# Kernel optimization log

Hardware: AMD Instinct MI355X
Metric: run time of the kernel (lower is better)

## Reference

```python
import jax, jax.numpy as jnp
import numpy as np

N_NODES = 100000
N_EDGES = 1600000
NIN = 128
NHID = 128
N_GRAPHS = 1024


def _gcn_conv(x, src, dst, norm, W, b, n_nodes):
    """PyG-style GCNConv: linear (no bias) -> normalized scatter-add -> + bias."""
    xw = x @ W                                   # [N, out]
    msg = xw[src] * norm[:, None]                # gather + edge-normalize, [E', out]
    out = jax.ops.segment_sum(msg, dst, num_segments=n_nodes)
    return out + b


def _gcn_norm(edge_index, n_nodes):
    """Add self-loops and compute symmetric deg^{-1/2} normalization per edge."""
    loops = jnp.arange(n_nodes, dtype=edge_index.dtype)
    src = jnp.concatenate([edge_index[0], loops])
    dst = jnp.concatenate([edge_index[1], loops])
    deg = jax.ops.segment_sum(jnp.ones_like(dst, dtype=jnp.float32), dst,
                              num_segments=n_nodes)
    deg_isqrt = jnp.where(deg > 0, jax.lax.rsqrt(jnp.maximum(deg, 1.0)), 0.0)
    norm = deg_isqrt[src] * deg_isqrt[dst]
    return src, dst, norm


def setup_inputs() -> dict:
    key = jax.random.key(0)
    ks = jax.random.split(key, 8)
    x = jax.random.normal(ks[0], (N_NODES, NIN), dtype=jnp.float32)
    edge_index = jax.random.randint(ks[1], (2, N_EDGES), 0, N_NODES, dtype=jnp.int64)
    batch = jnp.sort(jax.random.randint(ks[2], (N_NODES,), 0, N_GRAPHS, dtype=jnp.int64))
    s_in = 1.0 / np.sqrt(NIN)
    s_h = 1.0 / np.sqrt(NHID)
    return {
        "x": x,
        "edge_index": edge_index,
        "batch": batch,
        "W1": jax.random.normal(ks[3], (NIN, NHID), dtype=jnp.float32) * s_in,
        "b1": jnp.zeros((NHID,), dtype=jnp.float32),
        "W2": jax.random.normal(ks[4], (NHID, NHID), dtype=jnp.float32) * s_h,
        "b2": jnp.zeros((NHID,), dtype=jnp.float32),
        "W3": jax.random.normal(ks[5], (NHID, NHID), dtype=jnp.float32) * s_h,
        "b3": jnp.zeros((NHID,), dtype=jnp.float32),
        "Wfc": jax.random.normal(ks[6], (NHID, 1), dtype=jnp.float32) * s_h,
        "bfc": jnp.zeros((1,), dtype=jnp.float32),
    }


def reference(x, edge_index, batch, W1, b1, W2, b2, W3, b3, Wfc, bfc):
    n_nodes = x.shape[0]
    src, dst, norm = _gcn_norm(edge_index, n_nodes)
    h = jax.nn.relu(_gcn_conv(x, src, dst, norm, W1, b1, n_nodes))
    h = jax.nn.relu(_gcn_conv(h, src, dst, norm, W2, b2, n_nodes))
    h = jax.nn.relu(_gcn_conv(h, src, dst, norm, W3, b3, n_nodes))
    # global mean pool over graphs in the batch
    sums = jax.ops.segment_sum(h, batch, num_segments=N_GRAPHS)      # [G, NHID]
    cnts = jax.ops.segment_sum(jnp.ones((n_nodes,), dtype=h.dtype), batch,
                               num_segments=N_GRAPHS)
    pooled = sums / jnp.maximum(cnts, 1.0)[:, None]
    return pooled @ Wfc + bfc                                        # [G, 1]
```

## Files before the change

### kernel.cpp

```cpp
#include <hip/hip_runtime.h>

#define N_NODES   100000
#define N_EDGES   1600000
#define NFEAT     128
#define N_GRAPHS  1024

#define BSHIFT  8
#define BNODES  256
#define NBUCK   391
#define BCAP    4608
#define SC_EDGES 4096
#define SC_EPT   8
#define SC_BLOCKS 391
#define BD_EPT   18

#define WT_STRIDE 136
#define GEMM_BLOCKS 782

typedef unsigned int uint32;
typedef unsigned short ushort;
typedef __attribute__((ext_vector_type(8))) short short8;
typedef __attribute__((ext_vector_type(4))) float f32x4;

__device__ inline ushort f2b(float f) {
    uint32 x = __float_as_uint(f);
    uint32 r = x + 0x7fffu + ((x >> 16) & 1u);
    return (ushort)(r >> 16);
}
__device__ inline float blo(uint32 u) { return __uint_as_float(u << 16); }
__device__ inline float bhi(uint32 u) { return __uint_as_float(u & 0xffff0000u); }

__device__ inline short8 cvt8(const float* p) {
    float4 v0 = ((const float4*)p)[0];
    float4 v1 = ((const float4*)p)[1];
    short8 r;
    r[0] = (short)f2b(v0.x); r[1] = (short)f2b(v0.y);
    r[2] = (short)f2b(v0.z); r[3] = (short)f2b(v0.w);
    r[4] = (short)f2b(v1.x); r[5] = (short)f2b(v1.y);
    r[6] = (short)f2b(v1.z); r[7] = (short)f2b(v1.w);
    return r;
}

__global__ __launch_bounds__(256) void k_castw(const float* __restrict__ W1, const float* __restrict__ W2,
                                               const float* __restrict__ W3, ushort* __restrict__ WT,
                                               int* __restrict__ cur) {
    int i = blockIdx.x * blockDim.x + threadIdx.x;
    if (i < NBUCK) cur[i] = 0;
    if (i >= 3 * NFEAT * NFEAT) return;
    int l = i >> 14;
    int j = i & 16383;
    int n = j >> 7;
    int k = j & 127;
    const float* W = (l == 0) ? W1 : (l == 1) ? W2 : W3;
    WT[i] = f2b(W[k * NFEAT + n]);
}

struct SMemScatter {
    int hist[NBUCK], lofs[NBUCK], gbase[NBUCK];
    int wsum[4];
    uint32 sortedP[SC_EDGES];
    ushort sortedB[SC_EDGES];
};

__global__ __launch_bounds__(512) void k_phase1(const int* __restrict__ src, const int* __restrict__ dst,
                                                int* __restrict__ cur, uint32* __restrict__ bbuf,
                                                const float* __restrict__ A, const ushort* __restrict__ WTl,
                                                ushort* __restrict__ C, int M) {
    __shared__ __align__(16) char smem[NFEAT * WT_STRIDE * 2];
    int t = threadIdx.x;
    if (blockIdx.x < SC_BLOCKS) {
        SMemScatter& S = *(SMemScatter*)smem;
        int e0 = blockIdx.x * SC_EDGES;
        int total = N_EDGES - e0; if (total > SC_EDGES) total = SC_EDGES; if (total < 0) total = 0;
        for (int i = t; i < NBUCK; i += 512) S.hist[i] = 0;
        __syncthreads();
        uint32 val[SC_EPT];
        int    meta[SC_EPT];
        #pragma unroll
        for (int k = 0; k < SC_EPT; ++k) {
            int i = t + k * 512;
            meta[k] = -1;
            if (i < total) {
                int s = src[e0 + i], d = dst[e0 + i];
                int b = d >> BSHIFT;
                int tk = atomicAdd(&S.hist[b], 1);
                val[k] = ((uint32)(d & (BNODES - 1)) << 17) | (uint32)s;
                meta[k] = (b << 13) | tk;
            }
        }
        __syncthreads();
        int inc = 0, ts = 0, h0 = 0;
        if (t < 256) {
            int b0 = 2 * t, b1 = 2 * t + 1;
            h0 = (b0 < NBUCK) ? S.hist[b0] : 0;
            int h1 = (b1 < NBUCK) ? S.hist[b1] : 0;
            ts = h0 + h1;
            int lane = t & 63;
            inc = ts;
            #pragma unroll
            for (int d = 1; d < 64; d <<= 1) {
                int u = __shfl_up(inc, d, 64);
                if (lane >= d) inc += u;
            }
            if (lane == 63) S.wsum[t >> 6] = inc;
        }
        __syncthreads();
        if (t < 256) {
            int w = t >> 6;
            int wpre = 0;
            for (int i = 0; i < w; ++i) wpre += S.wsum[i];
            int run = wpre + inc - ts;
            int b0 = 2 * t, b1 = 2 * t + 1;
            int h1 = ts - h0;
            if (b0 < NBUCK) {
                S.lofs[b0] = run;
                if (h0) S.gbase[b0] = atomicAdd(&cur[b0], h0);
            }
            if (b1 < NBUCK) {
                S.lofs[b1] = run + h0;
                if (h1) S.gbase[b1] = atomicAdd(&cur[b1], h1);
            }
        }
        __syncthreads();
        #pragma unroll
        for (int k = 0; k < SC_EPT; ++k) {
            if (meta[k] >= 0) {
                int b = meta[k] >> 13;
                int p = S.lofs[b] + (meta[k] & 0x1FFF);
                S.sortedP[p] = val[k];
                S.sortedB[p] = (ushort)b;
            }
        }
        __syncthreads();
        for (int i = t; i < total; i += 512) {
            int b = S.sortedB[i];
            int addr = S.gbase[b] + (i - S.lofs[b]);
            if (addr < BCAP)
                bbuf[(size_t)b * BCAP + addr] = S.sortedP[i];
        }
    } else {
        ushort* sWT = (ushort*)smem;
        int gb = blockIdx.x - SC_BLOCKS;
        for (int i = t; i < NFEAT * 16; i += 512) {
            int n = i >> 4, c = i & 15;
            *(float4*)(sWT + n * WT_STRIDE + c * 8) = ((const float4*)WTl)[i];
        }
        int wave = t >> 6, lane = t & 63;
        int m0 = gb * 128 + wave * 16;
        int mRow = m0 + (lane & 15);
        if (mRow >= M) mRow = M - 1;
        int kg = lane >> 4;
        const float* Ap = A + (size_t)mRow * NFEAT + kg * 8;
        short8 a0 = cvt8(Ap);
        short8 a1 = cvt8(Ap + 32);
        short8 a2 = cvt8(Ap + 64);
        short8 a3 = cvt8(Ap + 96);
        __syncthreads();

        f32x4 acc[8];
        #pragma unroll
        for (int nt = 0; nt < 8; ++nt) acc[nt] = (f32x4){0.f, 0.f, 0.f, 0.f};
        #pragma unroll
        for (int nt = 0; nt < 8; ++nt) {
            int n = nt * 16 + (lane & 15);
            const short8* Bp = (const short8*)(sWT + n * WT_STRIDE + kg * 8);
            short8 b0 = Bp[0];
            short8 b1 = Bp[4];
            short8 b2 = Bp[8];
            short8 b3 = Bp[12];
            acc[nt] = __builtin_amdgcn_mfma_f32_16x16x32_bf16(a0, b0, acc[nt], 0, 0, 0);
            acc[nt] = __builtin_amdgcn_mfma_f32_16x16x32_bf16(a1, b1, acc[nt], 0, 0, 0);
            acc[nt] = __builtin_amdgcn_mfma_f32_16x16x32_bf16(a2, b2, acc[nt], 0, 0, 0);
            acc[nt] = __builtin_amdgcn_mfma_f32_16x16x32_bf16(a3, b3, acc[nt], 0, 0, 0);
        }
        __syncthreads();
        {
            int colBase = lane & 15;
            #pragma unroll
            for (int r = 0; r < 4; ++r) {
                int lr = wave * 16 + kg * 4 + r;
                #pragma unroll
                for (int nt = 0; nt < 8; ++nt)
                    sWT[lr * NFEAT + nt * 16 + colBase] = f2b(acc[nt][r]);
            }
        }
        __syncthreads();
        {
            int rowBase = gb * 128;
            const float4* sC4 = (const float4*)sWT;
            for (int i = t; i < 2048; i += 512) {
                int row = i >> 4;
                int gr = rowBase + row;
                if (gr < M) ((float4*)(C + (size_t)gr * NFEAT))[i & 15] = sC4[i];
            }
        }
    }
}

__global__ __launch_bounds__(256) void k_build(const uint32* __restrict__ bbuf, const int* __restrict__ cur,
                                               int* __restrict__ col, int* __restrict__ offsets,
                                               float* __restrict__ dinv) {
    int b = blockIdx.x;
    __shared__ int hist[BNODES], excl[BNODES];
    __shared__ int wsum[4], wtot[4];
    __shared__ int sorted[BCAP];
    __shared__ int sBase, sTotal;
    int t = threadIdx.x;
    {
        int pre = 0, tot = 0;
        #pragma unroll
        for (int q = 0; q < 2; ++q) {
            int i = 2 * t + q;
            if (i < NBUCK) {
                int v = cur[i]; if (v > BCAP) v = BCAP;
                tot += v;
                if (i < b) pre += v;
            }
        }
        int lane = t & 63, w = t >> 6;
        #pragma unroll
        for (int d = 32; d > 0; d >>= 1) { pre += __shfl_down(pre, d, 64); tot += __shfl_down(tot, d, 64); }
        if (lane == 0) { wsum[w] = pre; wtot[w] = tot; }
        __syncthreads();
        if (t == 0) {
            sBase = wsum[0] + wsum[1] + wsum[2] + wsum[3];
            sTotal = wtot[0] + wtot[1] + wtot[2] + wtot[3];
        }
        hist[t] = 0;
    }
    __syncthreads();
    int base = sBase;
    if (b == NBUCK - 1 && t == 0) offsets[N_NODES] = sTotal;
    int cnt = cur[b]; if (cnt > BCAP) cnt = BCAP;
    const uint32* reg = bbuf + (size_t)b * BCAP;

    uint32 val[BD_EPT];
    int    meta[BD_EPT];
    #pragma unroll
    for (int k = 0; k < BD_EPT; ++k) {
        int i = t + k * 256;
        meta[k] = -1;
        if (i < cnt) {
            uint32 p = reg[i];
            int node = p >> 17;
            int tk = atomicAdd(&hist[node], 1);
            val[k] = p & 0x1FFFF;
            meta[k] = (node << 16) | tk;
        }
    }
    __syncthreads();
    {
        int c = hist[t];
        int lane = t & 63, w = t >> 6;
        int inc = c;
        #pragma unroll
        for (int d = 1; d < 64; d <<= 1) {
            int u = __shfl_up(inc, d, 64);
            if (lane >= d) inc += u;
        }
        if (lane == 63) wsum[w] = inc;
        __syncthreads();
        int wpre = 0;
        for (int i = 0; i < w; ++i) wpre += wsum[i];
        int e = wpre + inc - c;
        excl[t] = e;
        int node = (b << BSHIFT) + t;
        if (node < N_NODES) {
            offsets[node] = base + e;
            dinv[node] = rsqrtf((float)(c + 1));
        }
    }
    __syncthreads();
    #pragma unroll
    for (int k = 0; k < BD_EPT; ++k) {
        if (meta[k] >= 0) {
            int node = meta[k] >> 16;
            sorted[excl[node] + (meta[k] & 0xFFFF)] = (int)val[k];
        }
    }
    __syncthreads();
    for (int i = t; i < cnt; i += 256) col[base + i] = sorted[i];
}

#define AGG_GROUP4 \
    int half = lane >> 4; \
    int fl = lane & 15; \
    float dn = dinv[n]; \
    int e0 = off[n], e1 = off[n + 1]; \
    int deg = e1 - e0; \
    int maxd = deg; \
    { int u16 = __shfl_xor(maxd, 16, 64); if (u16 > maxd) maxd = u16; \
      int u32 = __shfl_xor(maxd, 32, 64); if (u32 > maxd) maxd = u32; } \
    const uint4* XW4 = (const uint4*)XWu; \
    uint4 sv = XW4[(size_t)n * 16 + fl]; \
    float ws = dn * dn; \
    float a0 = ws * blo(sv.x), a1 = ws * bhi(sv.x); \
    float a2 = ws * blo(sv.y), a3 = ws * bhi(sv.y); \
    float a4 = ws * blo(sv.z), a5 = ws * bhi(sv.z); \
    float a6 = ws * blo(sv.w), a7 = ws * bhi(sv.w); \
    int cm = 0; float wm = 0.f; \
    if (fl < deg) { cm = col[e0 + fl]; wm = dn * dinv[cm]; } \
    for (int base = 0; base < maxd; base += 16) { \
        int nb = base + 16; \
        int cmn = 0; float wmn = 0.f; \
        if (nb + fl < deg) { cmn = col[e0 + nb + fl]; wmn = dn * dinv[cmn]; } \
        int lim = maxd - base; if (lim > 16) lim = 16; \
        for (int j = 0; j < lim; j += 8) { \
            uint4 u[8]; float w[8]; \
            _Pragma("unroll") \
            for (int p = 0; p < 8; ++p) { \
                int sl = (half << 4) + j + p; \
                int cc = __shfl(cm, sl, 64); \
                w[p] = __shfl(wm, sl, 64); \
                u[p] = XW4[(size_t)cc * 16 + fl]; \
            } \
            _Pragma("unroll") \
            for (int p = 0; p < 8; ++p) { \
                a0 = fmaf(w[p], blo(u[p].x), a0); a1 = fmaf(w[p], bhi(u[p].x), a1); \
                a2 = fmaf(w[p], blo(u[p].y), a2); a3 = fmaf(w[p], bhi(u[p].y), a3); \
                a4 = fmaf(w[p], blo(u[p].z), a4); a5 = fmaf(w[p], bhi(u[p].z), a5); \
                a6 = fmaf(w[p], blo(u[p].w), a6); a7 = fmaf(w[p], bhi(u[p].w), a7); \
            } \
        } \
        cm = cmn; wm = wmn; \
    }

__global__ __launch_bounds__(256) void k_agg_gemm(const uint32* __restrict__ XWu,
                                                  const int* __restrict__ col,
                                                  const int* __restrict__ off,
                                                  const float* __restrict__ dinv,
                                                  const float* __restrict__ bias,
                                                  const ushort* __restrict__ WTl,
                                                  ushort* __restrict__ C) {
    __shared__ __align__(16) ushort sA[16 * WT_STRIDE];
    int t = threadIdx.x;
    int lane = t & 63;
    int lw = t >> 6;
    int n = (blockIdx.x << 4) + (lw << 2) + (lane >> 4);
    AGG_GROUP4
    {
        float4 bb0 = ((const float4*)bias)[2 * fl];
        float4 bb1 = ((const float4*)bias)[2 * fl + 1];
        float r0 = fmaxf(a0 + bb0.x, 0.f), r1 = fmaxf(a1 + bb0.y, 0.f);
        float r2 = fmaxf(a2 + bb0.z, 0.f), r3 = fmaxf(a3 + bb0.w, 0.f);
        float r4 = fmaxf(a4 + bb1.x, 0.f), r5 = fmaxf(a5 + bb1.y, 0.f);
        float r6 = fmaxf(a6 + bb1.z, 0.f), r7 = fmaxf(a7 + bb1.w, 0.f);
        uint4 o;
        o.x = (uint32)f2b(r0) | ((uint32)f2b(r1) << 16);
        o.y = (uint32)f2b(r2) | ((uint32)f2b(r3) << 16);
        o.z = (uint32)f2b(r4) | ((uint32)f2b(r5) << 16);
        o.w = (uint32)f2b(r6) | ((uint32)f2b(r7) << 16);
        int lrow = (lw << 2) + half;
        *(uint4*)(sA + lrow * WT_STRIDE + fl * 8) = o;
    }
    __syncthreads();
    {
        const short8* Ap = (const short8*)(sA + fl * WT_STRIDE + half * 8);
        short8 af0 = Ap[0];
        short8 af1 = Ap[4];
        short8 af2 = Ap[8];
        short8 af3 = Ap[12];
        f32x4 acc[2];
        acc[0] = (f32x4){0.f, 0.f, 0.f, 0.f};
        acc[1] = (f32x4){0.f, 0.f, 0.f, 0.f};
        #pragma unroll
        for (int q = 0; q < 2; ++q) {
            int nt = lw * 2 + q;
            const short8* Bp = (const short8*)(WTl + (nt * 16 + fl) * NFEAT + half * 8);
            short8 b0 = Bp[0];
            short8 b1 = Bp[4];
            short8 b2 = Bp[8];
            short8 b3 = Bp[12];
            acc[q] = __builtin_amdgcn_mfma_f32_16x16x32_bf16(af0, b0, acc[q], 0, 0, 0);
            acc[q] = __builtin_amdgcn_mfma_f32_16x16x32_bf16(af1, b1, acc[q], 0, 0, 0);
            acc[q] = __builtin_amdgcn_mfma_f32_16x16x32_bf16(af2, b2, acc[q], 0, 0, 0);
            acc[q] = __builtin_amdgcn_mfma_f32_16x16x32_bf16(af3, b3, acc[q], 0, 0, 0);
        }
        __syncthreads();
        #pragma unroll
        for (int q = 0; q < 2; ++q) {
            int nt = lw * 2 + q;
            #pragma unroll
            for (int r = 0; r < 4; ++r)
                sA[(half * 4 + r) * NFEAT + nt * 16 + fl] = f2b(acc[q][r]);
        }
    }
    __syncthreads();
    {
        int row = t >> 4;
        float4 v = ((const float4*)sA)[t];
        ((float4*)(C + (size_t)((blockIdx.x << 4) + row) * NFEAT))[t & 15] = v;
    }
}

__global__ __launch_bounds__(256) void k_agg_fc(const uint32* __restrict__ XWu, const int* __restrict__ col,
                                                const int* __restrict__ off, const float* __restrict__ dinv,
                                                const float* __restrict__ bias, const float* __restrict__ Wfc,
                                                float* __restrict__ nodeS) {
    int wid = (blockIdx.x * blockDim.x + threadIdx.x) >> 6;
    int lane = threadIdx.x & 63;
    int n = (wid << 2) + (lane >> 4);
    if (n >= N_NODES) return;
    AGG_GROUP4
    float4 bb0 = ((const float4*)bias)[2 * fl];
    float4 bb1 = ((const float4*)bias)[2 * fl + 1];
    float4 wf0 = ((const float4*)Wfc)[2 * fl];
    float4 wf1 = ((const float4*)Wfc)[2 * fl + 1];
    float s = fmaxf(a0 + bb0.x, 0.f) * wf0.x + fmaxf(a1 + bb0.y, 0.f) * wf0.y
            + fmaxf(a2 + bb0.z, 0.f) * wf0.z + fmaxf(a3 + bb0.w, 0.f) * wf0.w
            + fmaxf(a4 + bb1.x, 0.f) * wf1.x + fmaxf(a5 + bb1.y, 0.f) * wf1.y
            + fmaxf(a6 + bb1.z, 0.f) * wf1.z + fmaxf(a7 + bb1.w, 0.f) * wf1.w;
    s += __shfl_xor(s, 8, 64);
    s += __shfl_xor(s, 4, 64);
    s += __shfl_xor(s, 2, 64);
    s += __shfl_xor(s, 1, 64);
    if (fl == 0) nodeS[n] = s;
}

__device__ inline int lower_bound_dev(const int* a, int n, int key) {
    int lo = 0, hi = n;
    while (lo < hi) {
        int mid = (lo + hi) >> 1;
        if (a[mid] < key) lo = mid + 1; else hi = mid;
    }
    return lo;
}

__global__ __launch_bounds__(256) void k_pool(const float* __restrict__ nodeS, const int* __restrict__ batch,
                                              const float* __restrict__ bfc, float* __restrict__ out) {
    int g = blockIdx.x;
    int t = threadIdx.x;
    int lo = lower_bound_dev(batch, N_NODES, g);
    int hi = lower_bound_dev(batch, N_NODES, g + 1);
    float s = 0.f;
    for (int i = lo + t; i < hi; i += 256) s += nodeS[i];
    for (int d = 32; d > 0; d >>= 1) s += __shfl_down(s, d, 64);
    __shared__ float ws[4];
    int lane = t & 63, w = t >> 6;
    if (lane == 0) ws[w] = s;
    __syncthreads();
    if (t == 0) {
        float tot = ws[0] + ws[1] + ws[2] + ws[3];
        float cnt = (float)(hi - lo);
        out[g] = tot / fmaxf(cnt, 1.0f) + bfc[0];
    }
}

extern "C" void kernel_launch(void* const* d_in, const int* in_sizes, int n_in,
                              void* d_out, int out_size, void* d_ws, size_t ws_size,
                              hipStream_t stream) {
    const float* x    = (const float*)d_in[0];
    const int*   ei   = (const int*)d_in[1];
    const int*   batch= (const int*)d_in[2];
    const float* W1   = (const float*)d_in[3];
    const float* b1   = (const float*)d_in[4];
    const float* W2   = (const float*)d_in[5];
    const float* b2   = (const float*)d_in[6];
    const float* W3   = (const float*)d_in[7];
    const float* b3   = (const float*)d_in[8];
    const float* Wfc  = (const float*)d_in[9];
    const float* bfc  = (const float*)d_in[10];
    float* out = (float*)d_out;

    const int* src = ei;
    const int* dst = ei + N_EDGES;

    char* p = (char*)d_ws;
    auto carve = [&](size_t bytes) { void* r = (void*)p; p += (bytes + 255) & ~(size_t)255; return r; };
    int*    cur       = (int*)   carve(sizeof(int) * NBUCK);
    uint32* bbuf      = (uint32*)carve(sizeof(uint32) * (size_t)NBUCK * BCAP);
    float*  dinv      = (float*) carve(sizeof(float) * N_NODES);
    int*    offsets   = (int*)   carve(sizeof(int) * (N_NODES + 1));
    int*    col       = (int*)   carve(sizeof(int) * N_EDGES);
    ushort* XW        = (ushort*)carve(sizeof(short) * (size_t)N_NODES * NFEAT);
    ushort* XW2       = (ushort*)carve(sizeof(short) * (size_t)N_NODES * NFEAT);
    ushort* WT        = (ushort*)carve(sizeof(short) * 3 * NFEAT * NFEAT);
    float*  nodeS     = (float*) carve(sizeof(float) * N_NODES);

    const int aggBlocks = N_NODES / 16;

    k_castw<<<(3 * NFEAT * NFEAT + 255) / 256, 256, 0, stream>>>(W1, W2, W3, WT, cur);
    k_phase1<<<SC_BLOCKS + GEMM_BLOCKS, 512, 0, stream>>>(src, dst, cur, bbuf, x, WT, XW, N_NODES);
    k_build<<<NBUCK, 256, 0, stream>>>(bbuf, cur, col, offsets, dinv);

    k_agg_gemm<<<aggBlocks, 256, 0, stream>>>((const uint32*)XW, col, offsets, dinv, b1,
                                              WT + NFEAT * NFEAT, XW2);
    k_agg_gemm<<<aggBlocks, 256, 0, stream>>>((const uint32*)XW2, col, offsets, dinv, b2,
                                              WT + 2 * NFEAT * NFEAT, XW);
    k_agg_fc<<<aggBlocks, 256, 0, stream>>>((const uint32*)XW, col, offsets, dinv, b3, Wfc, nodeS);

    k_pool<<<N_GRAPHS, 256, 0, stream>>>(nodeS, batch, bfc, out);
}
```

Baseline: 351.4 us.

## Replace bucketed two-pass CSR build with atomic degree count, scan and scatter

Builds the CSR adjacency a different way. The old path did a shared-memory bucket sort into a staging buffer followed by per-bucket local sorting. The new path counts degrees with global atomics, does a two-kernel prefix scan to get offsets and cursors, then places each edge with an atomic cursor increment. This removes the staging buffer, the shared-memory sorts and the capacity clamp. In exchange it adds random-address global atomics per edge, two more kernel launches, and a nondeterministic neighbor order within each node.

```diff
diff --git a/kernel.cpp b/kernel.cpp
--- a/kernel.cpp
+++ b/kernel.cpp
@@ -5,14 +5,10 @@
 #define NFEAT     128
 #define N_GRAPHS  1024
 
-#define BSHIFT  8
-#define BNODES  256
 #define NBUCK   391
-#define BCAP    4608
 #define SC_EDGES 4096
 #define SC_EPT   8
 #define SC_BLOCKS 391
-#define BD_EPT   18
 
 #define WT_STRIDE 136
 #define GEMM_BLOCKS 782
@@ -43,9 +39,9 @@
 
 __global__ __launch_bounds__(256) void k_castw(const float* __restrict__ W1, const float* __restrict__ W2,
                                                const float* __restrict__ W3, ushort* __restrict__ WT,
-                                               int* __restrict__ cur) {
+                                               int* __restrict__ deg) {
     int i = blockIdx.x * blockDim.x + threadIdx.x;
-    if (i < NBUCK) cur[i] = 0;
+    if (i < N_NODES) deg[i] = 0;
     if (i >= 3 * NFEAT * NFEAT) return;
     int l = i >> 14;
     int j = i & 16383;
@@ -55,91 +51,20 @@
     WT[i] = f2b(W[k * NFEAT + n]);
 }
 
-struct SMemScatter {
-    int hist[NBUCK], lofs[NBUCK], gbase[NBUCK];
-    int wsum[4];
-    uint32 sortedP[SC_EDGES];
-    ushort sortedB[SC_EDGES];
-};
-
 __global__ __launch_bounds__(512) void k_phase1(const int* __restrict__ src, const int* __restrict__ dst,
-                                                int* __restrict__ cur, uint32* __restrict__ bbuf,
+                                                int* __restrict__ deg,
                                                 const float* __restrict__ A, const ushort* __restrict__ WTl,
                                                 ushort* __restrict__ C, int M) {
-    __shared__ __align__(16) char smem[NFEAT * WT_STRIDE * 2];
+    __shared__ __align__(16) ushort sWT[NFEAT * WT_STRIDE];
     int t = threadIdx.x;
     if (blockIdx.x < SC_BLOCKS) {
-        SMemScatter& S = *(SMemScatter*)smem;
         int e0 = blockIdx.x * SC_EDGES;
-        int total = N_EDGES - e0; if (total > SC_EDGES) total = SC_EDGES; if (total < 0) total = 0;
-        for (int i = t; i < NBUCK; i += 512) S.hist[i] = 0;
-        __syncthreads();
-        uint32 val[SC_EPT];
-        int    meta[SC_EPT];
         #pragma unroll
         for (int k = 0; k < SC_EPT; ++k) {
-            int i = t + k * 512;
-            meta[k] = -1;
-            if (i < total) {
-                int s = src[e0 + i], d = dst[e0 + i];
-                int b = d >> BSHIFT;
-                int tk = atomicAdd(&S.hist[b], 1);
-                val[k] = ((uint32)(d & (BNODES - 1)) << 17) | (uint32)s;
-                meta[k] = (b << 13) | tk;
-            }
-        }
-        __syncthreads();
-        int inc = 0, ts = 0, h0 = 0;
-        if (t < 256) {
-            int b0 = 2 * t, b1 = 2 * t + 1;
-            h0 = (b0 < NBUCK) ? S.hist[b0] : 0;
-            int h1 = (b1 < NBUCK) ? S.hist[b1] : 0;
-            ts = h0 + h1;
-            int lane = t & 63;
-            inc = ts;
-            #pragma unroll
-            for (int d = 1; d < 64; d <<= 1) {
-                int u = __shfl_up(inc, d, 64);
-                if (lane >= d) inc += u;
-            }
-            if (lane == 63) S.wsum[t >> 6] = inc;
-        }
-        __syncthreads();
-        if (t < 256) {
-            int w = t >> 6;
-            int wpre = 0;
-            for (int i = 0; i < w; ++i) wpre += S.wsum[i];
-            int run = wpre + inc - ts;
-            int b0 = 2 * t, b1 = 2 * t + 1;
-            int h1 = ts - h0;
-            if (b0 < NBUCK) {
-                S.lofs[b0] = run;
-                if (h0) S.gbase[b0] = atomicAdd(&cur[b0], h0);
-            }
-            if (b1 < NBUCK) {
-                S.lofs[b1] = run + h0;
-                if (h1) S.gbase[b1] = atomicAdd(&cur[b1], h1);
-            }
-        }
-        __syncthreads();
-        #pragma unroll
-        for (int k = 0; k < SC_EPT; ++k) {
-            if (meta[k] >= 0) {
-                int b = meta[k] >> 13;
-                int p = S.lofs[b] + (meta[k] & 0x1FFF);
-                S.sortedP[p] = val[k];
-                S.sortedB[p] = (ushort)b;
-            }
-        }
-        __syncthreads();
-        for (int i = t; i < total; i += 512) {
-            int b = S.sortedB[i];
-            int addr = S.gbase[b] + (i - S.lofs[b]);
-            if (addr < BCAP)
-                bbuf[(size_t)b * BCAP + addr] = S.sortedP[i];
+            int i = e0 + t + k * 512;
+            if (i < N_EDGES) atomicAdd(&deg[dst[i]], 1);
         }
     } else {
-        ushort* sWT = (ushort*)smem;
         int gb = blockIdx.x - SC_BLOCKS;
         for (int i = t; i < NFEAT * 16; i += 512) {
             int n = i >> 4, c = i & 15;
@@ -197,89 +122,79 @@
     }
 }
 
-__global__ __launch_bounds__(256) void k_build(const uint32* __restrict__ bbuf, const int* __restrict__ cur,
-                                               int* __restrict__ col, int* __restrict__ offsets,
+__global__ __launch_bounds__(256) void k_scan1(const int* __restrict__ deg, int* __restrict__ bsum) {
+    int node = blockIdx.x * 256 + threadIdx.x;
+    int d = (node < N_NODES) ? deg[node] : 0;
+    int lane = threadIdx.x & 63, w = threadIdx.x >> 6;
+    #pragma unroll
+    for (int s = 32; s > 0; s >>= 1) d += __shfl_down(d, s, 64);
+    __shared__ int ws[4];
+    if (lane == 0) ws[w] = d;
+    __syncthreads();
+    if (threadIdx.x == 0) bsum[blockIdx.x] = ws[0] + ws[1] + ws[2] + ws[3];
+}
+
+__global__ __launch_bounds__(256) void k_scan2(const int* __restrict__ deg, const int* __restrict__ bsum,
+                                               int* __restrict__ offsets, int* __restrict__ cursor,
                                                float* __restrict__ dinv) {
-    int b = blockIdx.x;
-    __shared__ int hist[BNODES], excl[BNODES];
+    int b = blockIdx.x, t = threadIdx.x;
     __shared__ int wsum[4], wtot[4];
-    __shared__ int sorted[BCAP];
     __shared__ int sBase, sTotal;
-    int t = threadIdx.x;
+    int lane = t & 63, w = t >> 6;
     {
         int pre = 0, tot = 0;
         #pragma unroll
         for (int q = 0; q < 2; ++q) {
             int i = 2 * t + q;
             if (i < NBUCK) {
-                int v = cur[i]; if (v > BCAP) v = BCAP;
+                int v = bsum[i];
                 tot += v;
                 if (i < b) pre += v;
             }
         }
-        int lane = t & 63, w = t >> 6;
-        #pragma unroll
-        for (int d = 32; d > 0; d >>= 1) { pre += __shfl_down(pre, d, 64); tot += __shfl_down(tot, d, 64); }
+        #pragma unroll
+        for (int s = 32; s > 0; s >>= 1) { pre += __shfl_down(pre, s, 64); tot += __shfl_down(tot, s, 64); }
         if (lane == 0) { wsum[w] = pre; wtot[w] = tot; }
         __syncthreads();
         if (t == 0) {
             sBase = wsum[0] + wsum[1] + wsum[2] + wsum[3];
             sTotal = wtot[0] + wtot[1] + wtot[2] + wtot[3];
         }
-        hist[t] = 0;
-    }
-    __syncthreads();
-    int base = sBase;
+    }
+    __syncthreads();
+    int node = (b << 8) + t;
+    int c = (node < N_NODES) ? deg[node] : 0;
+    int inc = c;
+    #pragma unroll
+    for (int d2 = 1; d2 < 64; d2 <<= 1) {
+        int u = __shfl_up(inc, d2, 64);
+        if (lane >= d2) inc += u;
+    }
+    if (lane == 63) wsum[w] = inc;
+    __syncthreads();
+    int wpre = 0;
+    for (int i = 0; i < w; ++i) wpre += wsum[i];
+    int e = sBase + wpre + inc - c;
+    if (node < N_NODES) {
+        offsets[node] = e;
+        cursor[node]  = e;
+        dinv[node] = rsqrtf((float)(c + 1));
+    }
     if (b == NBUCK - 1 && t == 0) offsets[N_NODES] = sTotal;
-    int cnt = cur[b]; if (cnt > BCAP) cnt = BCAP;
-    const uint32* reg = bbuf + (size_t)b * BCAP;
-
-    uint32 val[BD_EPT];
-    int    meta[BD_EPT];
+}
+
+__global__ __launch_bounds__(512) void k_scatter(const int* __restrict__ src, const int* __restrict__ dst,
+                                                 int* __restrict__ cursor, int* __restrict__ col) {
+    int base = blockIdx.x * 2048;
     #pragma unroll
-    for (int k = 0; k < BD_EPT; ++k) {
-        int i = t + k * 256;
-        meta[k] = -1;
-        if (i < cnt) {
-            uint32 p = reg[i];
-            int node = p >> 17;
-            int tk = atomicAdd(&hist[node], 1);
-            val[k] = p & 0x1FFFF;
-            meta[k] = (node << 16) | tk;
-        }
-    }
-    __syncthreads();
-    {
-        int c = hist[t];
-        int lane = t & 63, w = t >> 6;
-        int inc = c;
-        #pragma unroll
-        for (int d = 1; d < 64; d <<= 1) {
-            int u = __shfl_up(inc, d, 64);
-            if (lane >= d) inc += u;
-        }
-        if (lane == 63) wsum[w] = inc;
-        __syncthreads();
-        int wpre = 0;
-        for (int i = 0; i < w; ++i) wpre += wsum[i];
-        int e = wpre + inc - c;
-        excl[t] = e;
-        int node = (b << BSHIFT) + t;
-        if (node < N_NODES) {
-            offsets[node] = base + e;
-            dinv[node] = rsqrtf((float)(c + 1));
-        }
-    }
-    __syncthreads();
-    #pragma unroll
-    for (int k = 0; k < BD_EPT; ++k) {
-        if (meta[k] >= 0) {
-            int node = meta[k] >> 16;
-            sorted[excl[node] + (meta[k] & 0xFFFF)] = (int)val[k];
-        }
-    }
-    __syncthreads();
-    for (int i = t; i < cnt; i += 256) col[base + i] = sorted[i];
+    for (int k = 0; k < 4; ++k) {
+        int i = base + k * 512 + threadIdx.x;
+        if (i < N_EDGES) {
+            int d = dst[i];
+            int pos = atomicAdd(&cursor[d], 1);
+            col[pos] = src[i];
+        }
+    }
 }
 
 #define AGG_GROUP4 \
@@ -467,8 +382,9 @@
 
     char* p = (char*)d_ws;
     auto carve = [&](size_t bytes) { void* r = (void*)p; p += (bytes + 255) & ~(size_t)255; return r; };
-    int*    cur       = (int*)   carve(sizeof(int) * NBUCK);
-    uint32* bbuf      = (uint32*)carve(sizeof(uint32) * (size_t)NBUCK * BCAP);
+    int*    deg       = (int*)   carve(sizeof(int) * N_NODES);
+    int*    bsum      = (int*)   carve(sizeof(int) * NBUCK);
+    int*    cursor    = (int*)   carve(sizeof(int) * N_NODES);
     float*  dinv      = (float*) carve(sizeof(float) * N_NODES);
     int*    offsets   = (int*)   carve(sizeof(int) * (N_NODES + 1));
     int*    col       = (int*)   carve(sizeof(int) * N_EDGES);
@@ -479,9 +395,11 @@
 
     const int aggBlocks = N_NODES / 16;
 
-    k_castw<<<(3 * NFEAT * NFEAT + 255) / 256, 256, 0, stream>>>(W1, W2, W3, WT, cur);
-    k_phase1<<<SC_BLOCKS + GEMM_BLOCKS, 512, 0, stream>>>(src, dst, cur, bbuf, x, WT, XW, N_NODES);
-    k_build<<<NBUCK, 256, 0, stream>>>(bbuf, cur, col, offsets, dinv);
+    k_castw<<<NBUCK, 256, 0, stream>>>(W1, W2, W3, WT, deg);
+    k_phase1<<<SC_BLOCKS + GEMM_BLOCKS, 512, 0, stream>>>(src, dst, deg, x, WT, XW, N_NODES);
+    k_scan1<<<NBUCK, 256, 0, stream>>>(deg, bsum);
+    k_scan2<<<NBUCK, 256, 0, stream>>>(deg, bsum, offsets, cursor, dinv);
+    k_scatter<<<GEMM_BLOCKS, 512, 0, stream>>>(src, dst, cursor, col);
 
     k_agg_gemm<<<aggBlocks, 256, 0, stream>>>((const uint32*)XW, col, offsets, dinv, b1,
                                               WT + NFEAT * NFEAT, XW2);
```

Measured after the change: 521.1 us. +48.3%, slower.

## Make the fused aggregate-GEMM per-wave using lane shuffles instead of block barriers

Applied to the files above, without the earlier changes.

Each wave now runs its own MFMA GEMM on its 4 aggregated rows. The bf16 rows are moved into MFMA A-fragments with cross-lane shuffles, and rows 4-15 of the 16-row tile are zero-padded. This removes the three block-wide __syncthreads, so waves finish their irregular gathers independently and do not wait on the slowest wave in the block. In exchange, each wave issues four times as many MFMAs, most of them on padding, and reloads the full weight matrix from global or cache itself.

```diff
diff --git a/kernel.cpp b/kernel.cpp
--- a/kernel.cpp
+++ b/kernel.cpp
@@ -332,12 +332,14 @@
                                                   const float* __restrict__ bias,
                                                   const ushort* __restrict__ WTl,
                                                   ushort* __restrict__ C) {
-    __shared__ __align__(16) ushort sA[16 * WT_STRIDE];
+    __shared__ __align__(16) ushort sC[4][4 * NFEAT];
     int t = threadIdx.x;
     int lane = t & 63;
     int lw = t >> 6;
-    int n = (blockIdx.x << 4) + (lw << 2) + (lane >> 4);
+    int wid = (blockIdx.x << 2) + lw;
+    int n = (wid << 2) + (lane >> 4);
     AGG_GROUP4
+    uint4 o;
     {
         float4 bb0 = ((const float4*)bias)[2 * fl];
         float4 bb1 = ((const float4*)bias)[2 * fl + 1];
@@ -345,51 +347,45 @@
         float r2 = fmaxf(a2 + bb0.z, 0.f), r3 = fmaxf(a3 + bb0.w, 0.f);
         float r4 = fmaxf(a4 + bb1.x, 0.f), r5 = fmaxf(a5 + bb1.y, 0.f);
         float r6 = fmaxf(a6 + bb1.z, 0.f), r7 = fmaxf(a7 + bb1.w, 0.f);
-        uint4 o;
         o.x = (uint32)f2b(r0) | ((uint32)f2b(r1) << 16);
         o.y = (uint32)f2b(r2) | ((uint32)f2b(r3) << 16);
         o.z = (uint32)f2b(r4) | ((uint32)f2b(r5) << 16);
         o.w = (uint32)f2b(r6) | ((uint32)f2b(r7) << 16);
-        int lrow = (lw << 2) + half;
-        *(uint4*)(sA + lrow * WT_STRIDE + fl * 8) = o;
-    }
-    __syncthreads();
-    {
-        const short8* Ap = (const short8*)(sA + fl * WT_STRIDE + half * 8);
-        short8 af0 = Ap[0];
-        short8 af1 = Ap[4];
-        short8 af2 = Ap[8];
-        short8 af3 = Ap[12];
-        f32x4 acc[2];
-        acc[0] = (f32x4){0.f, 0.f, 0.f, 0.f};
-        acc[1] = (f32x4){0.f, 0.f, 0.f, 0.f};
-        #pragma unroll
-        for (int q = 0; q < 2; ++q) {
-            int nt = lw * 2 + q;
-            const short8* Bp = (const short8*)(WTl + (nt * 16 + fl) * NFEAT + half * 8);
-            short8 b0 = Bp[0];
-            short8 b1 = Bp[4];
-            short8 b2 = Bp[8];
-            short8 b3 = Bp[12];
-            acc[q] = __builtin_amdgcn_mfma_f32_16x16x32_bf16(af0, b0, acc[q], 0, 0, 0);
-            acc[q] = __builtin_amdgcn_mfma_f32_16x16x32_bf16(af1, b1, acc[q], 0, 0, 0);
-            acc[q] = __builtin_amdgcn_mfma_f32_16x16x32_bf16(af2, b2, acc[q], 0, 0, 0);
-            acc[q] = __builtin_amdgcn_mfma_f32_16x16x32_bf16(af3, b3, acc[q], 0, 0, 0);
-        }
-        __syncthreads();
-        #pragma unroll
-        for (int q = 0; q < 2; ++q) {
-            int nt = lw * 2 + q;
+    }
+    int rowIdx = lane & 15;
+    int kg = lane >> 4;
+    f32x4 acc2[8];
+    #pragma unroll
+    for (int nt = 0; nt < 8; ++nt) acc2[nt] = (f32x4){0.f, 0.f, 0.f, 0.f};
+    #pragma unroll
+    for (int s = 0; s < 4; ++s) {
+        int srcLane = rowIdx * 16 + kg + s * 4;
+        union { int4 i; short8 h; } cvt;
+        cvt.i.x = __shfl((int)o.x, srcLane, 64);
+        cvt.i.y = __shfl((int)o.y, srcLane, 64);
+        cvt.i.z = __shfl((int)o.z, srcLane, 64);
+        cvt.i.w = __shfl((int)o.w, srcLane, 64);
+        if (rowIdx >= 4) { cvt.i.x = 0; cvt.i.y = 0; cvt.i.z = 0; cvt.i.w = 0; }
+        short8 af = cvt.h;
+        #pragma unroll
+        for (int nt = 0; nt < 8; ++nt) {
+            short8 bf = *(const short8*)(WTl + (nt * 16 + rowIdx) * NFEAT + s * 32 + kg * 8);
+            acc2[nt] = __builtin_amdgcn_mfma_f32_16x16x32_bf16(af, bf, acc2[nt], 0, 0, 0);
+        }
+    }
+    if (kg == 0) {
+        #pragma unroll
+        for (int nt = 0; nt < 8; ++nt) {
             #pragma unroll
             for (int r = 0; r < 4; ++r)
-                sA[(half * 4 + r) * NFEAT + nt * 16 + fl] = f2b(acc[q][r]);
-        }
-    }
-    __syncthreads();
+                sC[lw][r * NFEAT + nt * 16 + rowIdx] = f2b(acc2[nt][r]);
+        }
+    }
+    asm volatile("s_waitcnt lgkmcnt(0)" ::: "memory");
+    __builtin_amdgcn_sched_barrier(0);
     {
-        int row = t >> 4;
-        float4 v = ((const float4*)sA)[t];
-        ((float4*)(C + (size_t)((blockIdx.x << 4) + row) * NFEAT))[t & 15] = v;
+        uint4 v = *(const uint4*)&sC[lw][kg * NFEAT + rowIdx * 8];
+        ((uint4*)(C + (size_t)((wid << 2) + kg) * NFEAT))[rowIdx] = v;
     }
 }
 
```

New measurement: 514.2 us. 46.3% more time.
